# Performance work log

Measured on AMD Instinct MI355X. Metric: run time of the kernel, lower is better.

The kernel has to match this reference:

```python
import jax, jax.numpy as jnp
import numpy as np

B, D, H = 8192, 256, 1024


def setup_inputs() -> dict:
    key = jax.random.key(0)
    ks = jax.random.split(key, 24)
    glorot = lambda k, o, i: jax.random.uniform(k, (o, i), jnp.float32, -1.0, 1.0) * jnp.sqrt(6.0 / (o + i))
    inp = {
        'x': jax.random.normal(ks[0], (B, D), jnp.float32),
        'm': (jax.random.uniform(ks[1], (B, D)) < 0.8).astype(jnp.float32),  # binary observation mask
        'delta': jax.random.uniform(ks[2], (B, D), jnp.float32),             # nonnegative time gaps
        'h': jax.random.normal(ks[3], (B, H), jnp.float32),
        'x_last_obs': jax.random.normal(ks[4], (B, D), jnp.float32),
        'x_mean': jax.random.normal(ks[5], (D,), jnp.float32),
        'W_gamma_x': jax.random.uniform(ks[6], (D,), jnp.float32, 0.001, 0.01),
        'b_gamma_x': jnp.zeros((D,), jnp.float32),
        'W_gamma_h': glorot(ks[7], H, D), 'b_gamma_h': jnp.zeros((H,), jnp.float32),
        'W_xz': glorot(ks[8], H, D), 'W_hz': glorot(ks[9], H, H),
        'W_mz': glorot(ks[10], H, D), 'b_mz': jnp.zeros((H,), jnp.float32),
        'W_xr': glorot(ks[11], H, D), 'W_hr': glorot(ks[12], H, H),
        'W_mr': glorot(ks[13], H, D), 'b_mr': jnp.zeros((H,), jnp.float32),
        'W_xh': glorot(ks[14], H, D), 'W_hh': glorot(ks[15], H, H),
        'W_mh': glorot(ks[16], H, D), 'b_mh': jnp.zeros((H,), jnp.float32),
    }
    return inp


def reference(x, m, delta, h, x_last_obs, x_mean,
              W_gamma_x, b_gamma_x, W_gamma_h, b_gamma_h,
              W_xz, W_hz, W_mz, b_mz,
              W_xr, W_hr, W_mr, b_mr,
              W_xh, W_hh, W_mh, b_mh):
    # input decay (per-feature) and hidden decay (linear of delta)
    gamma_x = jnp.exp(-jax.nn.relu(delta * W_gamma_x + b_gamma_x))        # [B, D]
    gamma_h = jnp.exp(-jax.nn.relu(delta @ W_gamma_h.T + b_gamma_h))     # [B, H]
    # imputation
    x_last_obs_new = jnp.where(m > 0, x, x_last_obs)
    x_imputed = gamma_x * x_last_obs_new + (1.0 - gamma_x) * x_mean
    x_hat = m * x + (1.0 - m) * x_imputed
    h_decayed = gamma_h * h
    # GRU gates (eval mode: no recurrent dropout)
    z = jax.nn.sigmoid(x_hat @ W_xz.T + h_decayed @ W_hz.T + m @ W_mz.T + b_mz)
    r = jax.nn.sigmoid(x_hat @ W_xr.T + h_decayed @ W_hr.T + m @ W_mr.T + b_mr)
    h_tilde = jnp.tanh(x_hat @ W_xh.T + (r * h_decayed) @ W_hh.T + m @ W_mh.T + b_mh)
    h_new = (1.0 - z) * h_decayed + z * h_tilde
    return h_new, x_last_obs_new
```

## Files before the change

kernel.cpp:

```cpp
#include <hip/hip_runtime.h>
#include <cstdint>
#include <cstddef>

typedef unsigned short u16;
typedef __attribute__((ext_vector_type(8))) short s16x8;
typedef __attribute__((ext_vector_type(8))) u16 u16x8;
typedef __attribute__((ext_vector_type(4))) float f32x4;

#define DEV static __device__ __forceinline__
#define GPTR(p) (const __attribute__((address_space(1))) void*)(p)
#define LPTR(p) (__attribute__((address_space(3))) void*)(p)
#define SCHEDB __builtin_amdgcn_sched_barrier(0)
#define BAR __builtin_amdgcn_s_barrier()
#define SETP1 __builtin_amdgcn_s_setprio(1)
#define SETP0 __builtin_amdgcn_s_setprio(0)

DEV float b2f(u16 u) { union { unsigned i; float f; } c; c.i = ((unsigned)u) << 16; return c.f; }
DEV u16 f2b(float f) {
  union { float f; unsigned i; } c; c.f = f;
  unsigned r = (c.i + 0x7fffu + ((c.i >> 16) & 1u)) >> 16;
  return (u16)r;
}
DEV float sigm(float x) { return 1.0f / (1.0f + __expf(-x)); }

__global__ __launch_bounds__(256) void pack_w(
    const float* __restrict__ Wxz, const float* __restrict__ Whz, const float* __restrict__ Wmz,
    const float* __restrict__ Wxr, const float* __restrict__ Whr, const float* __restrict__ Wmr,
    const float* __restrict__ Wxh, const float* __restrict__ Whh, const float* __restrict__ Wmh,
    const float* __restrict__ Wgh,
    u16* __restrict__ WZR, u16* __restrict__ WH, u16* __restrict__ WGH)
{
  int t = blockIdx.x * 256 + threadIdx.x;
  const float* src;
  u16* dst;
  if (t < 589824) {
    int row = t / 192;
    int col = (t % 192) * 8;
    int rr = row & 1023;
    const float *wx, *wh, *wm;
    if (row < 1024)      { wx = Wxz; wh = Whz; wm = Wmz; }
    else if (row < 2048) { wx = Wxr; wh = Whr; wm = Wmr; }
    else                 { wx = Wxh; wh = Whh; wm = Wmh; }
    if (col < 256)       src = wx + rr * 256 + col;
    else if (col < 1280) src = wh + (size_t)rr * 1024 + (col - 256);
    else                 src = wm + rr * 256 + (col - 1280);
    dst = (row < 2048) ? (WZR + (size_t)row * 1536 + col)
                       : (WH + (size_t)(row - 2048) * 1536 + col);
  } else {
    int t2 = t - 589824;
    src = Wgh + t2 * 8;
    dst = WGH + t2 * 8;
  }
  f32x4 a = *(const f32x4*)src;
  f32x4 b = *(const f32x4*)(src + 4);
  u16x8 v;
#pragma unroll
  for (int j = 0; j < 4; ++j) { v[j] = f2b(a[j]); v[j + 4] = f2b(b[j]); }
  *(u16x8*)dst = v;
}

__global__ __launch_bounds__(256) void elem_k(
    const float* __restrict__ x, const float* __restrict__ m, const float* __restrict__ delta,
    const float* __restrict__ xlo, const float* __restrict__ x_mean,
    const float* __restrict__ Wgx, const float* __restrict__ bgx,
    u16* __restrict__ X1, u16* __restrict__ X2, u16* __restrict__ Dbf,
    float* __restrict__ out_xlo)
{
  int t = blockIdx.x * 256 + threadIdx.x;
  int row = t >> 5;
  int col = (t & 31) * 8;
  size_t base = (size_t)row * 256 + col;
  u16x8 vxhat, vm16, vd16;
  f32x4 vlnew[2];
#pragma unroll
  for (int half = 0; half < 2; ++half) {
    f32x4 vx = *(const f32x4*)(x + base + half * 4);
    f32x4 vm = *(const f32x4*)(m + base + half * 4);
    f32x4 vd = *(const f32x4*)(delta + base + half * 4);
    f32x4 vl = *(const f32x4*)(xlo + base + half * 4);
    f32x4 vmean = *(const f32x4*)(x_mean + col + half * 4);
    f32x4 vwg = *(const f32x4*)(Wgx + col + half * 4);
    f32x4 vbg = *(const f32x4*)(bgx + col + half * 4);
#pragma unroll
    for (int j = 0; j < 4; ++j) {
      float mf = vm[j];
      float lnew = (mf > 0.5f) ? vx[j] : vl[j];
      vlnew[half][j] = lnew;
      float gx = __expf(-fmaxf(vd[j] * vwg[j] + vbg[j], 0.0f));
      float ximp = gx * lnew + (1.0f - gx) * vmean[j];
      float xhat = mf * vx[j] + (1.0f - mf) * ximp;
      vxhat[half * 4 + j] = f2b(xhat);
      vm16[half * 4 + j] = f2b(mf);
      vd16[half * 4 + j] = f2b(vd[j]);
    }
  }
  size_t r1536 = (size_t)row * 1536;
  *(u16x8*)(X1 + r1536 + col) = vxhat;
  *(u16x8*)(X2 + r1536 + col) = vxhat;
  *(u16x8*)(X1 + r1536 + 1280 + col) = vm16;
  *(u16x8*)(X2 + r1536 + 1280 + col) = vm16;
  *(u16x8*)(Dbf + base) = vd16;
  *(f32x4*)(out_xlo + base) = vlnew[0];
  *(f32x4*)(out_xlo + base + 4) = vlnew[1];
}

__global__ __launch_bounds__(512, 4) void gemm_b256(
    const u16* __restrict__ A, const u16* __restrict__ W,
    const float* __restrict__ bz, const float* __restrict__ br,
    const u16* __restrict__ X1h, u16* __restrict__ Z, u16* __restrict__ X2)
{
  constexpr int K = 1536, P = 48;
  __shared__ alignas(16) u16 As[3][8192];
  __shared__ alignas(16) u16 Bs[3][4096];

  const int tid = threadIdx.x, lane = tid & 63, wave = tid >> 6;
  const int wr = wave >> 1, wc = wave & 1;
  const int d = blockIdx.x;
  const int L = (d & 7) * 64 + (d >> 3);
  const int brow = (L >> 4) * 256, bcol = (L & 15) * 128;
  const int lr = lane & 15, g4 = lane >> 4;
  const int rc = (g4 ^ ((lr >> 1) & 3)) * 8;
  const int srow = tid >> 2;
  const int scs = ((tid & 3) ^ ((srow >> 1) & 3)) * 8;

  f32x4 acc[4][4];
#pragma unroll
  for (int i = 0; i < 4; ++i)
#pragma unroll
    for (int j = 0; j < 4; ++j) { f32x4 z0 = {0.f, 0.f, 0.f, 0.f}; acc[i][j] = z0; }

  const u16* aP = A + (size_t)(brow + srow) * K + scs;
  const u16* aQ = aP + (size_t)128 * K;
  const u16* bP = W + (size_t)(bcol + srow) * K + scs;
  u16* dA = &As[0][0] + tid * 8;
  u16* dB = &Bs[0][0] + tid * 8;
  const u16* rA = &As[0][0] + (wr * 64 + lr) * 32 + rc;
  const u16* rB = &Bs[0][0] + (wc * 64 + lr) * 32 + rc;

  auto STAGE = [&](int slot, int ko) {
    __builtin_amdgcn_global_load_lds(GPTR(aP + ko), LPTR(dA + slot * 8192), 16, 0, 0);
    __builtin_amdgcn_global_load_lds(GPTR(aQ + ko), LPTR(dA + slot * 8192 + 4096), 16, 0, 0);
    __builtin_amdgcn_global_load_lds(GPTR(bP + ko), LPTR(dB + slot * 4096), 16, 0, 0);
  };

  STAGE(0, 0);
  STAGE(1, 32);
  asm volatile("s_waitcnt vmcnt(3)" ::: "memory");
  BAR;

#pragma unroll
  for (int u = 0; u < P; ++u) {
    const int sR = u % 3;
    const int sS = (u + 2) % 3;
    const int ko = ((u + 2 < P) ? (u + 2) : (P - 1)) * 32;
    s16x8 af[4], bf[4];
#pragma unroll
    for (int i = 0; i < 4; ++i) af[i] = *(const s16x8*)(rA + sR * 8192 + i * 512);
#pragma unroll
    for (int j = 0; j < 4; ++j) bf[j] = *(const s16x8*)(rB + sR * 4096 + j * 512);
    STAGE(sS, ko);
    SCHEDB;
    asm volatile("s_waitcnt vmcnt(3) lgkmcnt(0)" ::: "memory");
    SCHEDB;
    BAR;
    SETP1;
#pragma unroll
    for (int i = 0; i < 4; ++i)
#pragma unroll
      for (int j = 0; j < 4; ++j)
        acc[i][j] = __builtin_amdgcn_mfma_f32_16x16x32_bf16(af[i], bf[j], acc[i][j], 0, 0, 0);
    SETP0;
  }
  asm volatile("s_waitcnt vmcnt(0)" ::: "memory");

  const int row0 = brow + wr * 64 + g4 * 4;
  const int col0 = bcol + wc * 64 + lr;
#pragma unroll
  for (int i = 0; i < 4; ++i) {
#pragma unroll
    for (int j = 0; j < 4; ++j) {
      int c_ = col0 + j * 16;
#pragma unroll
      for (int qq = 0; qq < 4; ++qq) {
        int r_ = row0 + i * 16 + qq;
        float v = acc[i][j][qq];
        if (c_ < 1024) {
          Z[(size_t)r_ * 1024 + c_] = f2b(sigm(v + bz[c_]));
        } else {
          int jc = c_ - 1024;
          float rg = sigm(v + br[jc]);
          float hd = b2f(X1h[(size_t)r_ * 1536 + 256 + jc]);
          X2[(size_t)r_ * 1536 + 256 + jc] = f2b(rg * hd);
        }
      }
    }
  }
}

template<int EPI, int GXL>
__global__ __launch_bounds__(512, 4) void gemm_bt(
    const u16* __restrict__ A, int K, const u16* __restrict__ W,
    const float* __restrict__ bias0, const float* __restrict__ bias1,
    const float* __restrict__ auxf,
    const u16* __restrict__ auxb,
    const u16* __restrict__ aux2b,
    u16* __restrict__ out0b,
    float* __restrict__ outf)
{
  constexpr int GX = 1 << GXL;
  constexpr int SL = 128 * 32;
  __shared__ alignas(16) u16 As[4][SL];
  __shared__ alignas(16) u16 Bs[4][SL];

  const int tid = threadIdx.x;
  const int lane = tid & 63;
  const int wave = tid >> 6;
  const int wr = wave >> 2, wc = wave & 3;

  const int d = blockIdx.x;
  const int q = (int)gridDim.x >> 3;
  const int L = (d & 7) * q + (d >> 3);
  const int brow = (L >> GXL) * 128;
  const int bcol = (L & (GX - 1)) * 128;
  const int NT = K / 64;

  const int lr = lane & 15, g4 = lane >> 4;
  const int rc = (g4 ^ ((lr >> 1) & 3)) * 8;
  const int srow = lane >> 2;
  const int scs = ((lane & 3) ^ ((srow >> 1) & 3)) * 8;

  f32x4 acc[4][2];
#pragma unroll
  for (int i = 0; i < 4; ++i)
#pragma unroll
    for (int j = 0; j < 2; ++j) { f32x4 z0 = {0.f, 0.f, 0.f, 0.f}; acc[i][j] = z0; }

  const u16* aP = A + (size_t)(brow + wave * 16 + srow) * K + scs;
  const u16* bP = W + (size_t)(bcol + wave * 16 + srow) * K + scs;
  u16* ldsA = &As[0][0] + wave * 512;
  u16* ldsB = &Bs[0][0] + wave * 512;
  const u16* rdA = &As[0][0] + (wr * 64 + lr) * 32 + rc;
  const u16* rdB = &Bs[0][0] + (wc * 32 + lr) * 32 + rc;

  auto STAGE = [&](int slot, int koff) {
    __builtin_amdgcn_global_load_lds(GPTR(aP + koff), LPTR(ldsA + slot * SL), 16, 0, 0);
    __builtin_amdgcn_global_load_lds(GPTR(bP + koff), LPTR(ldsB + slot * SL), 16, 0, 0);
  };

  auto PHASE = [&](int slotR, int slotS, int koff, int stg, int vm) {
    s16x8 af[4], bf[2];
    const u16* pA = rdA + slotR * SL;
    const u16* pB = rdB + slotR * SL;
#pragma unroll
    for (int i = 0; i < 4; ++i) af[i] = *(const s16x8*)(pA + i * 512);
#pragma unroll
    for (int j = 0; j < 2; ++j) bf[j] = *(const s16x8*)(pB + j * 512);
    if (stg) STAGE(slotS, koff);
    SCHEDB;
    if (vm == 2) asm volatile("s_waitcnt vmcnt(2)" ::: "memory");
    else if (vm == 0) asm volatile("s_waitcnt vmcnt(0)" ::: "memory");
    BAR;
    asm volatile("s_waitcnt lgkmcnt(0)" ::: "memory");
    SCHEDB;
    SETP1;
#pragma unroll
    for (int i = 0; i < 4; ++i)
#pragma unroll
      for (int j = 0; j < 2; ++j)
        acc[i][j] = __builtin_amdgcn_mfma_f32_16x16x32_bf16(af[i], bf[j], acc[i][j], 0, 0, 0);
    SETP0;
  };

  STAGE(0, 0);
  STAGE(1, 32);
  asm volatile("s_waitcnt vmcnt(2)" ::: "memory");
  BAR;

  for (int kt = 0; kt < NT - 2; kt += 2) {
    PHASE(0, 2, 64, 1, 2);
    PHASE(1, 3, 96, 1, 2);
    PHASE(2, 0, 128, 1, 2);
    PHASE(3, 1, 160, 1, 2);
    aP += 128; bP += 128;
  }
  PHASE(0, 2, 64, 1, 2);
  PHASE(1, 3, 96, 1, 2);
  PHASE(2, 0, 0, 0, 0);
  PHASE(3, 0, 0, 0, -1);

  const int row0 = brow + wr * 64 + g4 * 4;
  const int col0 = bcol + wc * 32 + lr;
#pragma unroll
  for (int i = 0; i < 4; ++i) {
#pragma unroll
    for (int j = 0; j < 2; ++j) {
      int c_ = col0 + j * 16;
#pragma unroll
      for (int qq = 0; qq < 4; ++qq) {
        int r_ = row0 + i * 16 + qq;
        float v = acc[i][j][qq];
        if constexpr (EPI == 0) {
          float p = v + bias0[c_];
          float gh = __expf(-fmaxf(p, 0.0f));
          float hd = gh * auxf[(size_t)r_ * 1024 + c_];
          out0b[(size_t)r_ * 1536 + 256 + c_] = f2b(hd);
        } else {
          float ht = tanhf(v + bias0[c_]);
          float zz = b2f(aux2b[(size_t)r_ * 1024 + c_]);
          float hd = b2f(auxb[(size_t)r_ * 1536 + 256 + c_]);
          outf[(size_t)r_ * 1024 + c_] = (1.0f - zz) * hd + zz * ht;
        }
      }
    }
  }
}

extern "C" void kernel_launch(void* const* d_in, const int* in_sizes, int n_in,
                              void* d_out, int out_size, void* d_ws, size_t ws_size,
                              hipStream_t stream)
{
  const float* x     = (const float*)d_in[0];
  const float* m     = (const float*)d_in[1];
  const float* delta = (const float*)d_in[2];
  const float* h     = (const float*)d_in[3];
  const float* xlo   = (const float*)d_in[4];
  const float* xmean = (const float*)d_in[5];
  const float* Wgx   = (const float*)d_in[6];
  const float* bgx   = (const float*)d_in[7];
  const float* Wgh   = (const float*)d_in[8];
  const float* bgh   = (const float*)d_in[9];
  const float* Wxz   = (const float*)d_in[10];
  const float* Whz   = (const float*)d_in[11];
  const float* Wmz   = (const float*)d_in[12];
  const float* bmz   = (const float*)d_in[13];
  const float* Wxr   = (const float*)d_in[14];
  const float* Whr   = (const float*)d_in[15];
  const float* Wmr   = (const float*)d_in[16];
  const float* bmr   = (const float*)d_in[17];
  const float* Wxh   = (const float*)d_in[18];
  const float* Whh   = (const float*)d_in[19];
  const float* Wmh   = (const float*)d_in[20];
  const float* bmh   = (const float*)d_in[21];

  u16* X1  = (u16*)d_ws;
  u16* X2  = X1 + (size_t)8192 * 1536;
  u16* Z   = X2 + (size_t)8192 * 1536;
  u16* WZR = Z  + (size_t)8192 * 1024;
  u16* WH  = WZR + (size_t)2048 * 1536;
  u16* Dbf = WH + (size_t)1024 * 1536;
  u16* WGH = Dbf + (size_t)8192 * 256;

  float* out_h   = (float*)d_out;
  float* out_xlo = out_h + (size_t)8192 * 1024;

  pack_w<<<2432, 256, 0, stream>>>(Wxz, Whz, Wmz, Wxr, Whr, Wmr, Wxh, Whh, Wmh, Wgh, WZR, WH, WGH);
  elem_k<<<1024, 256, 0, stream>>>(x, m, delta, xlo, xmean, Wgx, bgx, X1, X2, Dbf, out_xlo);
  gemm_bt<0, 3><<<512, 512, 0, stream>>>(
      Dbf, 256, WGH, bgh, nullptr, h, nullptr, nullptr, X1, nullptr);
  gemm_b256<<<512, 512, 0, stream>>>(X1, WZR, bmz, bmr, X1, Z, X2);
  gemm_bt<2, 3><<<512, 512, 0, stream>>>(
      X2, 1536, WH, bmh, nullptr, nullptr, X1, Z, nullptr, out_h);
}
```

Measured before the change: 153.6 us.

## Enlarge z/r gate GEMM tile to 256x256 with split-phase LDS pipeline

The fused z/r gate GEMM now uses 256x256 output tiles per block instead of 256x128, halving the grid to 256 blocks. Each wave computes a 128x64 sub-tile in two halves. The K loop is restructured into interleaved A/B half-stage loads across two double-buffered 64-wide K chunks, overlapping LDS reads with MFMA. This raises arithmetic intensity and cuts redundant global traffic for A, at the cost of more registers, lower occupancy (launch bounds 2), and fewer blocks than CUs, which may leave some CUs idle.

Result: slower. 164.2 us (+6.9%).

```diff
diff --git a/kernel.cpp b/kernel.cpp
--- a/kernel.cpp
+++ b/kernel.cpp
@@ -104,79 +104,111 @@
   *(f32x4*)(out_xlo + base + 4) = vlnew[1];
 }
 
-__global__ __launch_bounds__(512, 4) void gemm_b256(
+__global__ __launch_bounds__(512, 2) void gemm_b256(
     const u16* __restrict__ A, const u16* __restrict__ W,
     const float* __restrict__ bz, const float* __restrict__ br,
     const u16* __restrict__ X1h, u16* __restrict__ Z, u16* __restrict__ X2)
 {
-  constexpr int K = 1536, P = 48;
-  __shared__ alignas(16) u16 As[3][8192];
-  __shared__ alignas(16) u16 Bs[3][4096];
+  constexpr int K = 1536, NT = 24;
+  __shared__ alignas(16) u16 As[4][8192];
+  __shared__ alignas(16) u16 Bs[4][8192];
 
   const int tid = threadIdx.x, lane = tid & 63, wave = tid >> 6;
-  const int wr = wave >> 1, wc = wave & 1;
+  const int wr = wave >> 2, wc = wave & 3;
   const int d = blockIdx.x;
-  const int L = (d & 7) * 64 + (d >> 3);
-  const int brow = (L >> 4) * 256, bcol = (L & 15) * 128;
+  const int L = (d & 7) * 32 + (d >> 3);
+  const int brow = (L >> 3) * 256, bcol = (L & 7) * 256;
   const int lr = lane & 15, g4 = lane >> 4;
   const int rc = (g4 ^ ((lr >> 1) & 3)) * 8;
   const int srow = tid >> 2;
   const int scs = ((tid & 3) ^ ((srow >> 1) & 3)) * 8;
 
-  f32x4 acc[4][4];
-#pragma unroll
-  for (int i = 0; i < 4; ++i)
+  f32x4 acc[8][4];
+#pragma unroll
+  for (int i = 0; i < 8; ++i)
 #pragma unroll
     for (int j = 0; j < 4; ++j) { f32x4 z0 = {0.f, 0.f, 0.f, 0.f}; acc[i][j] = z0; }
 
   const u16* aP = A + (size_t)(brow + srow) * K + scs;
   const u16* aQ = aP + (size_t)128 * K;
   const u16* bP = W + (size_t)(bcol + srow) * K + scs;
+  const u16* bQ = bP + (size_t)128 * K;
   u16* dA = &As[0][0] + tid * 8;
   u16* dB = &Bs[0][0] + tid * 8;
-  const u16* rA = &As[0][0] + (wr * 64 + lr) * 32 + rc;
-  const u16* rB = &Bs[0][0] + (wc * 64 + lr) * 32 + rc;
-
-  auto STAGE = [&](int slot, int ko) {
-    __builtin_amdgcn_global_load_lds(GPTR(aP + ko), LPTR(dA + slot * 8192), 16, 0, 0);
-    __builtin_amdgcn_global_load_lds(GPTR(aQ + ko), LPTR(dA + slot * 8192 + 4096), 16, 0, 0);
-    __builtin_amdgcn_global_load_lds(GPTR(bP + ko), LPTR(dB + slot * 4096), 16, 0, 0);
-  };
-
-  STAGE(0, 0);
-  STAGE(1, 32);
-  asm volatile("s_waitcnt vmcnt(3)" ::: "memory");
+  const u16* rA = &As[0][0] + lr * 32 + rc;
+  const u16* rB = &Bs[0][0] + lr * 32 + rc;
+
+  auto SA = [&](int so, int ko) {
+    __builtin_amdgcn_global_load_lds(GPTR(aP + ko), LPTR(dA + so), 16, 0, 0);
+    __builtin_amdgcn_global_load_lds(GPTR(aQ + ko), LPTR(dA + so + 4096), 16, 0, 0);
+  };
+  auto SB = [&](int so, int ko) {
+    __builtin_amdgcn_global_load_lds(GPTR(bP + ko), LPTR(dB + so), 16, 0, 0);
+    __builtin_amdgcn_global_load_lds(GPTR(bQ + ko), LPTR(dB + so + 4096), 16, 0, 0);
+  };
+
+  s16x8 afA[4], afB[4], bf0[4], bf1[4];
+  auto RDA = [&](s16x8* dst, int base, int rh) {
+#pragma unroll
+    for (int i = 0; i < 4; ++i)
+      dst[i] = *(const s16x8*)(rA + base + (wr * 128 + rh + i * 16) * 32);
+  };
+  auto RDB = [&](s16x8* dst, int base) {
+#pragma unroll
+    for (int j = 0; j < 4; ++j)
+      dst[j] = *(const s16x8*)(rB + base + (wc * 64 + j * 16) * 32);
+  };
+  auto MM = [&](s16x8* a, s16x8* b, int half) {
+    SETP1;
+#pragma unroll
+    for (int i = 0; i < 4; ++i)
+#pragma unroll
+      for (int j = 0; j < 4; ++j)
+        acc[half * 4 + i][j] = __builtin_amdgcn_mfma_f32_16x16x32_bf16(
+            a[i], b[j], acc[half * 4 + i][j], 0, 0, 0);
+    SETP0;
+  };
+
+  SA(0, 0);     SB(0, 0);
+  SA(8192, 32); SB(8192, 32);
+  asm volatile("s_waitcnt vmcnt(4)" ::: "memory");
   BAR;
-
-#pragma unroll
-  for (int u = 0; u < P; ++u) {
-    const int sR = u % 3;
-    const int sS = (u + 2) % 3;
-    const int ko = ((u + 2 < P) ? (u + 2) : (P - 1)) * 32;
-    s16x8 af[4], bf[4];
-#pragma unroll
-    for (int i = 0; i < 4; ++i) af[i] = *(const s16x8*)(rA + sR * 8192 + i * 512);
-#pragma unroll
-    for (int j = 0; j < 4; ++j) bf[j] = *(const s16x8*)(rB + sR * 4096 + j * 512);
-    STAGE(sS, ko);
-    SCHEDB;
-    asm volatile("s_waitcnt vmcnt(3) lgkmcnt(0)" ::: "memory");
-    SCHEDB;
-    BAR;
-    SETP1;
-#pragma unroll
-    for (int i = 0; i < 4; ++i)
-#pragma unroll
-      for (int j = 0; j < 4; ++j)
-        acc[i][j] = __builtin_amdgcn_mfma_f32_16x16x32_bf16(af[i], bf[j], acc[i][j], 0, 0, 0);
-    SETP0;
+  RDB(bf0, 0); RDA(afA, 0, 0);
+
+  for (int t = 0; t < NT; ++t) {
+    const int ro = (t & 1) << 14;
+    const int so = ro ^ 16384;
+    const int ko = (t + 1 < NT) ? 64 : 0;
+    RDA(afB, ro, 64);
+    SA(so, ko);
+    MM(afA, bf0, 0);
+    SCHEDB;
+    asm volatile("s_waitcnt vmcnt(2)" ::: "memory");
+    BAR;
+    RDB(bf1, ro + 8192); RDA(afA, ro + 8192, 0);
+    SB(so, ko);
+    MM(afB, bf0, 1);
+    SCHEDB;
+    BAR;
+    RDA(afB, ro + 8192, 64);
+    SA(so + 8192, ko + 32);
+    MM(afA, bf1, 0);
+    SCHEDB;
+    asm volatile("s_waitcnt vmcnt(2)" ::: "memory");
+    BAR;
+    if (t + 1 < NT) { RDB(bf0, so); RDA(afA, so, 0); }
+    SB(so + 8192, ko + 32);
+    MM(afB, bf1, 1);
+    SCHEDB;
+    BAR;
+    aP += 64; aQ += 64; bP += 64; bQ += 64;
   }
   asm volatile("s_waitcnt vmcnt(0)" ::: "memory");
 
-  const int row0 = brow + wr * 64 + g4 * 4;
+  const int row0 = brow + wr * 128 + g4 * 4;
   const int col0 = bcol + wc * 64 + lr;
 #pragma unroll
-  for (int i = 0; i < 4; ++i) {
+  for (int i = 0; i < 8; ++i) {
 #pragma unroll
     for (int j = 0; j < 4; ++j) {
       int c_ = col0 + j * 16;
@@ -357,7 +389,7 @@
   elem_k<<<1024, 256, 0, stream>>>(x, m, delta, xlo, xmean, Wgx, bgx, X1, X2, Dbf, out_xlo);
   gemm_bt<0, 3><<<512, 512, 0, stream>>>(
       Dbf, 256, WGH, bgh, nullptr, h, nullptr, nullptr, X1, nullptr);
-  gemm_b256<<<512, 512, 0, stream>>>(X1, WZR, bmz, bmr, X1, Z, X2);
+  gemm_b256<<<256, 512, 0, stream>>>(X1, WZR, bmz, bmr, X1, Z, X2);
   gemm_bt<2, 3><<<512, 512, 0, stream>>>(
       X2, 1536, WH, bmh, nullptr, nullptr, X1, Z, nullptr, out_h);
 }
```
